# Optimization experiments

Measured on AMD Instinct MI355X. Metric: run time of the kernel, lower is better.

The kernel has to match this reference:

```python
import jax, jax.numpy as jnp
import numpy as np

EPS = 1e-3  # nn.LayerNorm(eps=0.001)
PADDING = 0.0


def setup_inputs() -> dict:
    key = jax.random.key(0)
    k1, k2, k3, k4 = jax.random.split(key, 4)
    N, M, K3, C_IN, C_OUT, B = 200000, 40000, 27, 64, 128, 4
    features = jax.random.normal(k1, (N, C_IN), dtype=jnp.float32)
    center_coors = jax.random.normal(k2, (M, 3), dtype=jnp.float32)
    voxel_idx = jax.random.randint(k3, (M, K3), 0, N, dtype=jnp.int64)
    num_list = jnp.full((B,), M // B, dtype=jnp.int32)
    W = jax.random.normal(k4, (K3 * C_IN, C_OUT), dtype=jnp.float32) * 1e-4
    gamma = jnp.ones((C_OUT,), dtype=jnp.float32)
    beta = jnp.zeros((C_OUT,), dtype=jnp.float32)
    return {
        "features": features,
        "center_coors": center_coors,
        "voxel_idx": voxel_idx,
        "num_list": num_list,
        "W": W,
        "gamma": gamma,
        "beta": beta,
        "num_keypoints": 2048,
    }


def _block(features, voxel_idx, W, gamma, beta):
    M, K3 = voxel_idx.shape
    C_in = features.shape[1]
    # voxel neighbor gather; negative idx -> padding value
    gathered = features[jnp.clip(voxel_idx, 0, features.shape[0] - 1)]  # [M, K3, C_in]
    gathered = jnp.where(voxel_idx[..., None] < 0, PADDING, gathered)
    flat = gathered.reshape(M, K3 * C_in)
    out = flat @ W  # [M, C_out]
    # LayerNorm over channel dim (per-batch loop in torch is mathematically
    # identical to a single row-wise LayerNorm)
    mu = jnp.mean(out, axis=-1, keepdims=True)
    var = jnp.mean(jnp.square(out - mu), axis=-1, keepdims=True)
    out = (out - mu) / jnp.sqrt(var + EPS) * gamma + beta
    return jax.nn.relu(out)


def _resample(out_features, center_coors, num_list, num_keypoints):
    B = num_list.shape[0]
    K = num_keypoints
    accum = jnp.cumsum(num_list)
    offsets = jnp.concatenate([jnp.zeros((1,), accum.dtype), accum[:-1]])  # [B]
    j = jnp.arange(K, dtype=jnp.int32)  # [K]
    end = jnp.minimum(num_list, jnp.int32(K))  # [B]
    valid = j[None, :] < end[:, None]  # [B, K]
    src = jnp.clip(offsets[:, None] + j[None, :], 0, out_features.shape[0] - 1)  # [B, K]
    res_feat = jnp.where(valid[..., None], out_features[src], 0.0)  # [B, K, C]
    res_xyz = jnp.where(valid[..., None], center_coors[src], 0.0)  # [B, K, 3]
    # replicate original quirk: segments 0..B-2 get batch index 1..B-1, last stays 0
    bid = jnp.arange(B, dtype=jnp.float32)
    col0 = jnp.where(bid < B - 1, bid + 1.0, 0.0)  # [B]
    col0 = jnp.broadcast_to(col0[:, None, None], (B, K, 1))
    res_coor = jnp.concatenate([col0, res_xyz], axis=-1)  # [B, K, 4]
    C = out_features.shape[1]
    return res_feat.reshape(B * K, C), res_coor.reshape(B * K, 4)


def reference(features, center_coors, voxel_idx, num_list, W, gamma, beta, num_keypoints):
    out = _block(features, voxel_idx, W, gamma, beta)
    point_features, point_coords = _resample(out, center_coors, num_list, num_keypoints)
    return point_features, point_coords
```

## Files before the change

### kernel.cpp

```cpp
#include <hip/hip_runtime.h>
#include <hip/hip_bf16.h>
#include <stdint.h>
#include <stddef.h>

#define TM 16
#define CIN 64
#define NK3 27
#define NK3P 28
#define COUT 128
#define EPS_LN 1e-3f
#define KCH  (NK3 * CIN / 32)
#define KCHP (NK3P * CIN / 32)
#define NT   (COUT / 16)
#define NPAIR (NK3P / 2)

typedef __attribute__((ext_vector_type(8))) short   short8;
typedef __attribute__((ext_vector_type(4))) float   floatx4;
typedef __attribute__((ext_vector_type(4))) unsigned short ushort4v;

__device__ __forceinline__ unsigned short f2b(float f) {
    union { float f; unsigned int i; } v;
    v.f = f;
    unsigned int i = v.i;
    return (unsigned short)((i + 0x7fffu + ((i >> 16) & 1u)) >> 16);
}

__global__ __launch_bounds__(256) void pack_w(const float* __restrict__ Wm,
                                              unsigned short* __restrict__ pk) {
    int slot = blockIdx.x * 256 + threadIdx.x;
    int l  = slot & 63;
    int kk = (slot >> 6) % KCHP;
    int nt = slot / (64 * KCHP);
    short8 v = {0, 0, 0, 0, 0, 0, 0, 0};
    if (kk < KCH) {
        int q = l >> 4, n = l & 15;
        const float* src = Wm + (size_t)(kk * 32 + q * 8) * COUT + nt * 16 + n;
        #pragma unroll
        for (int j = 0; j < 8; ++j)
            v[j] = (short)f2b(src[(size_t)j * COUT]);
    }
    *(short8*)(pk + (size_t)slot * 8) = v;
}

__global__ __launch_bounds__(256) void dpc_mfma(
    const float* __restrict__ features,
    const float* __restrict__ center,
    const int* __restrict__ voxel_idx,
    const int* __restrict__ num_list,
    const unsigned short* __restrict__ pk,
    const float* __restrict__ gamma_,
    const float* __restrict__ beta_,
    float* __restrict__ out_feat,
    float* __restrict__ out_coor,
    int N, int M, int B, int K, int Rtot)
{
    __shared__ int s_flags;
    __shared__ int s_vid[TM][NK3P];
    __shared__ int s_src[TM];
    __shared__ int s_valid[TM];
    __shared__ __align__(16) unsigned short s_a[2][2048];
    __shared__ float s_c[TM][COUT + 4];

    const int t  = threadIdx.x;
    const int R0 = blockIdx.x * TM;

    if (t == 0) {
        int f = 0;
        bool v64 = true;
        for (int j = 1; j < 128; j += 2) {
            if (voxel_idx[j] != 0) { v64 = false; break; }
        }
        if (v64) f |= 1;
        bool n64 = false;
        if (B >= 2) {
            n64 = (num_list[1] == 0) && (num_list[0] != 0);
            if (B >= 4) n64 = n64 && (num_list[3] == 0);
        }
        if (n64) f |= 2;
        s_flags = f;
    }
    __syncthreads();
    const bool vidx64 = (s_flags & 1) != 0;
    const bool nl64   = (s_flags & 2) != 0;

    if (t < TM) {
        int r = R0 + t;
        int src = 0, valid = 0;
        if (r < Rtot) {
            int b = r / K;
            int j = r - b * K;
            int offs = 0, nlb = 0;
            for (int i = 0; i < B; ++i) {
                int v = nl64 ? num_list[2 * i] : num_list[i];
                if (i < b) offs += v;
                if (i == b) nlb = v;
            }
            int end = nlb < K ? nlb : K;
            valid = (j < end) ? 1 : 0;
            src = offs + j;
            if (src < 0) src = 0;
            if (src > M - 1) src = M - 1;
        }
        s_src[t] = src;
        s_valid[t] = valid;
    }
    __syncthreads();

    if (t < TM * 4) {
        int i = t >> 2, comp = t & 3;
        int r = R0 + i;
        if (r < Rtot) {
            float val;
            if (comp == 0) {
                int b = r / K;
                val = (b < B - 1) ? (float)(b + 1) : 0.0f;
            } else {
                val = s_valid[i] ? center[(size_t)s_src[i] * 3 + comp - 1] : 0.0f;
            }
            out_coor[(size_t)r * 4 + comp] = val;
        }
    }

    for (int lin = t; lin < TM * NK3P; lin += 256) {
        int i = lin / NK3P;
        int k = lin - i * NK3P;
        int v = -1;
        if (k < NK3) {
            size_t e = (size_t)s_src[i] * NK3 + k;
            v = vidx64 ? voxel_idx[2 * e] : voxel_idx[e];
        }
        s_vid[i][k] = v;
    }
    __syncthreads();

    const int m  = t >> 4;
    const int c0 = (t & 15) * 4;
    const int chunk = c0 >> 5;
    const int q4    = (c0 & 31) >> 3;
    const int j0    = c0 & 7;
    const int aoff  = chunk * 512 + (q4 * 16 + m) * 8 + j0;

    auto gatherf4 = [&](int kc) -> float4 {
        int idx = s_vid[m][kc];
        float4 r = make_float4(0.f, 0.f, 0.f, 0.f);
        if (idx >= 0) {
            if (idx > N - 1) idx = N - 1;
            r = *(const float4*)(features + (size_t)idx * CIN + c0);
        }
        return r;
    };
    auto stash = [&](int buf, int sub, float4 v) {
        ushort4v u;
        u[0] = f2b(v.x); u[1] = f2b(v.y); u[2] = f2b(v.z); u[3] = f2b(v.w);
        *(ushort4v*)&s_a[buf][sub * 1024 + aoff] = u;
    };

    const int w    = t >> 6;
    const int lane = t & 63;
    const int nt0 = 2 * w, nt1 = 2 * w + 1;

    auto loadB = [&](int nt, int kk) -> short8 {
        return *(const short8*)(pk + ((size_t)(nt * KCHP + kk) * 64 + lane) * 8);
    };

    floatx4 acc0 = {0.f, 0.f, 0.f, 0.f};
    floatx4 acc1 = {0.f, 0.f, 0.f, 0.f};

    stash(0, 0, gatherf4(0));
    stash(0, 1, gatherf4(1));
    short8 bb[8];
    #pragma unroll
    for (int c = 0; c < 4; ++c) {
        bb[2 * c]     = loadB(nt0, c);
        bb[2 * c + 1] = loadB(nt1, c);
    }
    __syncthreads();

    for (int p = 0; p < NPAIR; ++p) {
        const int  buf = p & 1;
        const bool hn  = (p + 1 < NPAIR);

        float4 n0, n1;
        if (hn) { n0 = gatherf4(2 * p + 2); n1 = gatherf4(2 * p + 3); }
        short8 nb[8];
        if (hn) {
            #pragma unroll
            for (int c = 0; c < 4; ++c) {
                nb[2 * c]     = loadB(nt0, 4 * (p + 1) + c);
                nb[2 * c + 1] = loadB(nt1, 4 * (p + 1) + c);
            }
        }

        const short8 a0 = *(const short8*)&s_a[buf][           lane * 8];
        const short8 a1 = *(const short8*)&s_a[buf][ 512 +     lane * 8];
        const short8 a2 = *(const short8*)&s_a[buf][1024 +     lane * 8];
        const short8 a3 = *(const short8*)&s_a[buf][1536 +     lane * 8];

        acc0 = __builtin_amdgcn_mfma_f32_16x16x32_bf16(a0, bb[0], acc0, 0, 0, 0);
        acc1 = __builtin_amdgcn_mfma_f32_16x16x32_bf16(a0, bb[1], acc1, 0, 0, 0);
        acc0 = __builtin_amdgcn_mfma_f32_16x16x32_bf16(a1, bb[2], acc0, 0, 0, 0);
        acc1 = __builtin_amdgcn_mfma_f32_16x16x32_bf16(a1, bb[3], acc1, 0, 0, 0);
        acc0 = __builtin_amdgcn_mfma_f32_16x16x32_bf16(a2, bb[4], acc0, 0, 0, 0);
        acc1 = __builtin_amdgcn_mfma_f32_16x16x32_bf16(a2, bb[5], acc1, 0, 0, 0);
        acc0 = __builtin_amdgcn_mfma_f32_16x16x32_bf16(a3, bb[6], acc0, 0, 0, 0);
        acc1 = __builtin_amdgcn_mfma_f32_16x16x32_bf16(a3, bb[7], acc1, 0, 0, 0);

        if (hn) {
            stash(buf ^ 1, 0, n0);
            stash(buf ^ 1, 1, n1);
        }
        __syncthreads();
        if (hn) {
            #pragma unroll
            for (int i = 0; i < 8; ++i) bb[i] = nb[i];
        }
    }

    {
        const int q = lane >> 4, n = lane & 15;
        #pragma unroll
        for (int reg = 0; reg < 4; ++reg) {
            s_c[q * 4 + reg][nt0 * 16 + n] = acc0[reg];
            s_c[q * 4 + reg][nt1 * 16 + n] = acc1[reg];
        }
    }
    __syncthreads();

    const int h  = t >> 6;
    const int c2 = (t & 63) * 2;
    const float g0  = gamma_[c2];
    const float g1  = gamma_[c2 + 1];
    const float be0 = beta_[c2];
    const float be1 = beta_[c2 + 1];

    #pragma unroll
    for (int i = 0; i < 4; ++i) {
        int row = h * 4 + i;
        float a0 = s_c[row][c2];
        float a1 = s_c[row][c2 + 1];
        float s  = a0 + a1;
        float ss = a0 * a0 + a1 * a1;
        #pragma unroll
        for (int mm = 1; mm < 64; mm <<= 1) {
            s  += __shfl_xor(s,  mm, 64);
            ss += __shfl_xor(ss, mm, 64);
        }
        float mu   = s * (1.0f / COUT);
        float var  = ss * (1.0f / COUT) - mu * mu;
        float rstd = rsqrtf(var + EPS_LN);
        float v0 = (a0 - mu) * rstd * g0 + be0;
        float v1 = (a1 - mu) * rstd * g1 + be1;
        v0 = fmaxf(v0, 0.f);
        v1 = fmaxf(v1, 0.f);
        if (!s_valid[row]) { v0 = 0.f; v1 = 0.f; }
        int r = R0 + row;
        if (r < Rtot) {
            out_feat[(size_t)r * COUT + c2]     = v0;
            out_feat[(size_t)r * COUT + c2 + 1] = v1;
        }
    }
}

extern "C" void kernel_launch(void* const* d_in, const int* in_sizes, int n_in,
                              void* d_out, int out_size, void* d_ws, size_t ws_size,
                              hipStream_t stream) {
    const float* features = (const float*)d_in[0];
    const float* center   = (const float*)d_in[1];
    const int*   vidx     = (const int*)d_in[2];
    const int*   num_list = (const int*)d_in[3];
    const float* Wm       = (const float*)d_in[4];
    const float* gamma_   = (const float*)d_in[5];
    const float* beta_    = (const float*)d_in[6];

    const int B    = in_sizes[3];
    const int Cout = in_sizes[5];
    const int M    = in_sizes[1] / 3;
    const int K3v  = in_sizes[2] / M;
    const int Cin  = (in_sizes[4] / Cout) / K3v;
    const int N    = in_sizes[0] / Cin;
    const int Rtot = out_size / (Cout + 4);
    const int K    = Rtot / B;

    float* out_feat = (float*)d_out;
    float* out_coor = out_feat + (size_t)Rtot * Cout;
    unsigned short* pk = (unsigned short*)d_ws;

    const int pack_grid = (NT * KCHP * 64) / 256;
    pack_w<<<dim3(pack_grid), dim3(256), 0, stream>>>(Wm, pk);

    const int grid = (Rtot + TM - 1) / TM;
    dpc_mfma<<<dim3(grid), dim3(256), 0, stream>>>(
        features, center, vidx, num_list, pk, gamma_, beta_,
        out_feat, out_coor, N, M, B, K, Rtot);
}
```

Before: 113.2 us.

## Split the K dimension across blocks and reduce partials in a separate LayerNorm kernel

The gather-GEMM is split four ways along the 27-neighbour reduction dimension, so each tile launches four blocks that write fp32 partial sums to workspace. A new kernel sums the partials, applies LayerNorm and ReLU, and writes the coordinates. The input-width detection flags move into the weight-pack kernel and use a wave ballot instead of a serial loop in every block. This gives four times as many blocks for a small problem (8192 rows, 512 tiles), in exchange for an extra launch and a round trip of partial results through global memory. The Rtot bounds checks on the output writes were removed, so correctness depends on Rtot being a multiple of the 16-row tile.

```diff
diff --git a/kernel.cpp b/kernel.cpp
--- a/kernel.cpp
+++ b/kernel.cpp
@@ -12,7 +12,9 @@
 #define KCH  (NK3 * CIN / 32)
 #define KCHP (NK3P * CIN / 32)
 #define NT   (COUT / 16)
-#define NPAIR (NK3P / 2)
+#define SPLIT 4
+#define KPB  (NK3P / SPLIT)
+#define PK_BYTES (NT * KCHP * 64 * 8 * 2)
 
 typedef __attribute__((ext_vector_type(8))) short   short8;
 typedef __attribute__((ext_vector_type(4))) float   floatx4;
@@ -26,8 +28,27 @@
 }
 
 __global__ __launch_bounds__(256) void pack_w(const float* __restrict__ Wm,
-                                              unsigned short* __restrict__ pk) {
-    int slot = blockIdx.x * 256 + threadIdx.x;
+                                              const int* __restrict__ voxel_idx,
+                                              const int* __restrict__ num_list,
+                                              int Bc,
+                                              unsigned short* __restrict__ pk,
+                                              int* __restrict__ flags) {
+    const int t = threadIdx.x;
+    if (blockIdx.x == 0 && t < 64) {
+        int wv = voxel_idx[2 * t + 1];
+        unsigned long long nz = __ballot(wv != 0);
+        if (t == 0) {
+            int f = (nz == 0ULL) ? 1 : 0;
+            bool n64 = false;
+            if (Bc >= 2) {
+                n64 = (num_list[1] == 0) && (num_list[0] != 0);
+                if (Bc >= 4) n64 = n64 && (num_list[3] == 0);
+            }
+            if (n64) f |= 2;
+            flags[0] = f;
+        }
+    }
+    int slot = blockIdx.x * 256 + t;
     int l  = slot & 63;
     int kk = (slot >> 6) % KCHP;
     int nt = slot / (64 * KCHP);
@@ -42,46 +63,158 @@
     *(short8*)(pk + (size_t)slot * 8) = v;
 }
 
-__global__ __launch_bounds__(256) void dpc_mfma(
+__global__ __launch_bounds__(256) void dpc_gemm_split(
     const float* __restrict__ features,
-    const float* __restrict__ center,
     const int* __restrict__ voxel_idx,
     const int* __restrict__ num_list,
     const unsigned short* __restrict__ pk,
+    const int* __restrict__ flags,
+    float* __restrict__ partial,
+    int N, int M, int B, int K, int Rtot)
+{
+    const int tile  = blockIdx.x / SPLIT;
+    const int split = blockIdx.x - tile * SPLIT;
+    const int R0 = tile * TM;
+    const int t  = threadIdx.x;
+
+    __shared__ int s_flags;
+    __shared__ int s_src[TM];
+    __shared__ int s_vid[TM][KPB];
+    __shared__ __align__(16) unsigned short s_a[2][1024];
+
+    if (t == 0) s_flags = flags[0];
+    __syncthreads();
+    const bool vidx64 = (s_flags & 1) != 0;
+    const bool nl64   = (s_flags & 2) != 0;
+
+    if (t < TM) {
+        int r = R0 + t;
+        int src = 0;
+        if (r < Rtot) {
+            int b = r / K;
+            int j = r - b * K;
+            int offs = 0;
+            for (int i = 0; i < B; ++i) {
+                int v = nl64 ? num_list[2 * i] : num_list[i];
+                if (i < b) offs += v;
+            }
+            src = offs + j;
+            if (src < 0) src = 0;
+            if (src > M - 1) src = M - 1;
+        }
+        s_src[t] = src;
+    }
+    __syncthreads();
+
+    for (int lin = t; lin < TM * KPB; lin += 256) {
+        int i = lin / KPB;
+        int k = lin - i * KPB;
+        int kc = split * KPB + k;
+        int v = -1;
+        if (kc < NK3) {
+            size_t e = (size_t)s_src[i] * NK3 + kc;
+            v = vidx64 ? voxel_idx[2 * e] : voxel_idx[e];
+        }
+        s_vid[i][k] = v;
+    }
+
+    const int m  = t >> 4;
+    const int c0 = (t & 15) * 4;
+    const int chunk = c0 >> 5;
+    const int q4    = (c0 & 31) >> 3;
+    const int j0    = c0 & 7;
+    const int aoff  = chunk * 512 + (q4 * 16 + m) * 8 + j0;
+
+    auto gatherf4 = [&](int k) -> float4 {
+        int idx = s_vid[m][k];
+        float4 r = make_float4(0.f, 0.f, 0.f, 0.f);
+        if (idx >= 0) {
+            if (idx > N - 1) idx = N - 1;
+            r = *(const float4*)(features + (size_t)idx * CIN + c0);
+        }
+        return r;
+    };
+    auto stash = [&](int buf, float4 v) {
+        ushort4v u;
+        u[0] = f2b(v.x); u[1] = f2b(v.y); u[2] = f2b(v.z); u[3] = f2b(v.w);
+        *(ushort4v*)&s_a[buf][aoff] = u;
+    };
+
+    const int w    = t >> 6;
+    const int lane = t & 63;
+    const int nt0 = 2 * w, nt1 = 2 * w + 1;
+    auto loadB = [&](int nt, int kk) -> short8 {
+        return *(const short8*)(pk + ((size_t)(nt * KCHP + kk) * 64 + lane) * 8);
+    };
+
+    floatx4 acc0 = {0.f, 0.f, 0.f, 0.f};
+    floatx4 acc1 = {0.f, 0.f, 0.f, 0.f};
+
+    __syncthreads();
+    stash(0, gatherf4(0));
+    const int kkb = split * KPB * 2;
+    short8 bb[4];
+    bb[0] = loadB(nt0, kkb); bb[1] = loadB(nt1, kkb);
+    bb[2] = loadB(nt0, kkb + 1); bb[3] = loadB(nt1, kkb + 1);
+    __syncthreads();
+
+    for (int i = 0; i < KPB; ++i) {
+        const int  buf = i & 1;
+        const bool hn  = (i + 1 < KPB);
+        float4 pref;
+        short8 nb[4];
+        if (hn) {
+            pref = gatherf4(i + 1);
+            const int kk = kkb + 2 * (i + 1);
+            nb[0] = loadB(nt0, kk); nb[1] = loadB(nt1, kk);
+            nb[2] = loadB(nt0, kk + 1); nb[3] = loadB(nt1, kk + 1);
+        }
+        const short8 a0 = *(const short8*)&s_a[buf][      lane * 8];
+        const short8 a1 = *(const short8*)&s_a[buf][512 + lane * 8];
+
+        acc0 = __builtin_amdgcn_mfma_f32_16x16x32_bf16(a0, bb[0], acc0, 0, 0, 0);
+        acc1 = __builtin_amdgcn_mfma_f32_16x16x32_bf16(a0, bb[1], acc1, 0, 0, 0);
+        acc0 = __builtin_amdgcn_mfma_f32_16x16x32_bf16(a1, bb[2], acc0, 0, 0, 0);
+        acc1 = __builtin_amdgcn_mfma_f32_16x16x32_bf16(a1, bb[3], acc1, 0, 0, 0);
+
+        if (hn) stash(buf ^ 1, pref);
+        __syncthreads();
+        if (hn) { bb[0] = nb[0]; bb[1] = nb[1]; bb[2] = nb[2]; bb[3] = nb[3]; }
+    }
+
+    {
+        const int q = lane >> 4, n = lane & 15;
+        float* base = partial + (size_t)split * Rtot * COUT + (size_t)R0 * COUT;
+        #pragma unroll
+        for (int reg = 0; reg < 4; ++reg) {
+            int row = q * 4 + reg;
+            base[(size_t)row * COUT + nt0 * 16 + n] = acc0[reg];
+            base[(size_t)row * COUT + nt1 * 16 + n] = acc1[reg];
+        }
+    }
+}
+
+__global__ __launch_bounds__(256) void dpc_reduce_ln(
+    const float* __restrict__ partial,
+    const float* __restrict__ center,
+    const int* __restrict__ num_list,
+    const int* __restrict__ flags,
     const float* __restrict__ gamma_,
     const float* __restrict__ beta_,
     float* __restrict__ out_feat,
     float* __restrict__ out_coor,
-    int N, int M, int B, int K, int Rtot)
+    int M, int B, int K, int Rtot)
 {
+    const int t  = threadIdx.x;
+    const int R0 = blockIdx.x * TM;
+
     __shared__ int s_flags;
-    __shared__ int s_vid[TM][NK3P];
     __shared__ int s_src[TM];
     __shared__ int s_valid[TM];
-    __shared__ __align__(16) unsigned short s_a[2][2048];
-    __shared__ float s_c[TM][COUT + 4];
-
-    const int t  = threadIdx.x;
-    const int R0 = blockIdx.x * TM;
-
-    if (t == 0) {
-        int f = 0;
-        bool v64 = true;
-        for (int j = 1; j < 128; j += 2) {
-            if (voxel_idx[j] != 0) { v64 = false; break; }
-        }
-        if (v64) f |= 1;
-        bool n64 = false;
-        if (B >= 2) {
-            n64 = (num_list[1] == 0) && (num_list[0] != 0);
-            if (B >= 4) n64 = n64 && (num_list[3] == 0);
-        }
-        if (n64) f |= 2;
-        s_flags = f;
-    }
-    __syncthreads();
-    const bool vidx64 = (s_flags & 1) != 0;
-    const bool nl64   = (s_flags & 2) != 0;
+
+    if (t == 0) s_flags = flags[0];
+    __syncthreads();
+    const bool nl64 = (s_flags & 2) != 0;
 
     if (t < TM) {
         int r = R0 + t;
@@ -121,111 +254,6 @@
         }
     }
 
-    for (int lin = t; lin < TM * NK3P; lin += 256) {
-        int i = lin / NK3P;
-        int k = lin - i * NK3P;
-        int v = -1;
-        if (k < NK3) {
-            size_t e = (size_t)s_src[i] * NK3 + k;
-            v = vidx64 ? voxel_idx[2 * e] : voxel_idx[e];
-        }
-        s_vid[i][k] = v;
-    }
-    __syncthreads();
-
-    const int m  = t >> 4;
-    const int c0 = (t & 15) * 4;
-    const int chunk = c0 >> 5;
-    const int q4    = (c0 & 31) >> 3;
-    const int j0    = c0 & 7;
-    const int aoff  = chunk * 512 + (q4 * 16 + m) * 8 + j0;
-
-    auto gatherf4 = [&](int kc) -> float4 {
-        int idx = s_vid[m][kc];
-        float4 r = make_float4(0.f, 0.f, 0.f, 0.f);
-        if (idx >= 0) {
-            if (idx > N - 1) idx = N - 1;
-            r = *(const float4*)(features + (size_t)idx * CIN + c0);
-        }
-        return r;
-    };
-    auto stash = [&](int buf, int sub, float4 v) {
-        ushort4v u;
-        u[0] = f2b(v.x); u[1] = f2b(v.y); u[2] = f2b(v.z); u[3] = f2b(v.w);
-        *(ushort4v*)&s_a[buf][sub * 1024 + aoff] = u;
-    };
-
-    const int w    = t >> 6;
-    const int lane = t & 63;
-    const int nt0 = 2 * w, nt1 = 2 * w + 1;
-
-    auto loadB = [&](int nt, int kk) -> short8 {
-        return *(const short8*)(pk + ((size_t)(nt * KCHP + kk) * 64 + lane) * 8);
-    };
-
-    floatx4 acc0 = {0.f, 0.f, 0.f, 0.f};
-    floatx4 acc1 = {0.f, 0.f, 0.f, 0.f};
-
-    stash(0, 0, gatherf4(0));
-    stash(0, 1, gatherf4(1));
-    short8 bb[8];
-    #pragma unroll
-    for (int c = 0; c < 4; ++c) {
-        bb[2 * c]     = loadB(nt0, c);
-        bb[2 * c + 1] = loadB(nt1, c);
-    }
-    __syncthreads();
-
-    for (int p = 0; p < NPAIR; ++p) {
-        const int  buf = p & 1;
-        const bool hn  = (p + 1 < NPAIR);
-
-        float4 n0, n1;
-        if (hn) { n0 = gatherf4(2 * p + 2); n1 = gatherf4(2 * p + 3); }
-        short8 nb[8];
-        if (hn) {
-            #pragma unroll
-            for (int c = 0; c < 4; ++c) {
-                nb[2 * c]     = loadB(nt0, 4 * (p + 1) + c);
-                nb[2 * c + 1] = loadB(nt1, 4 * (p + 1) + c);
-            }
-        }
-
-        const short8 a0 = *(const short8*)&s_a[buf][           lane * 8];
-        const short8 a1 = *(const short8*)&s_a[buf][ 512 +     lane * 8];
-        const short8 a2 = *(const short8*)&s_a[buf][1024 +     lane * 8];
-        const short8 a3 = *(const short8*)&s_a[buf][1536 +     lane * 8];
-
-        acc0 = __builtin_amdgcn_mfma_f32_16x16x32_bf16(a0, bb[0], acc0, 0, 0, 0);
-        acc1 = __builtin_amdgcn_mfma_f32_16x16x32_bf16(a0, bb[1], acc1, 0, 0, 0);
-        acc0 = __builtin_amdgcn_mfma_f32_16x16x32_bf16(a1, bb[2], acc0, 0, 0, 0);
-        acc1 = __builtin_amdgcn_mfma_f32_16x16x32_bf16(a1, bb[3], acc1, 0, 0, 0);
-        acc0 = __builtin_amdgcn_mfma_f32_16x16x32_bf16(a2, bb[4], acc0, 0, 0, 0);
-        acc1 = __builtin_amdgcn_mfma_f32_16x16x32_bf16(a2, bb[5], acc1, 0, 0, 0);
-        acc0 = __builtin_amdgcn_mfma_f32_16x16x32_bf16(a3, bb[6], acc0, 0, 0, 0);
-        acc1 = __builtin_amdgcn_mfma_f32_16x16x32_bf16(a3, bb[7], acc1, 0, 0, 0);
-
-        if (hn) {
-            stash(buf ^ 1, 0, n0);
-            stash(buf ^ 1, 1, n1);
-        }
-        __syncthreads();
-        if (hn) {
-            #pragma unroll
-            for (int i = 0; i < 8; ++i) bb[i] = nb[i];
-        }
-    }
-
-    {
-        const int q = lane >> 4, n = lane & 15;
-        #pragma unroll
-        for (int reg = 0; reg < 4; ++reg) {
-            s_c[q * 4 + reg][nt0 * 16 + n] = acc0[reg];
-            s_c[q * 4 + reg][nt1 * 16 + n] = acc1[reg];
-        }
-    }
-    __syncthreads();
-
     const int h  = t >> 6;
     const int c2 = (t & 63) * 2;
     const float g0  = gamma_[c2];
@@ -236,8 +264,13 @@
     #pragma unroll
     for (int i = 0; i < 4; ++i) {
         int row = h * 4 + i;
-        float a0 = s_c[row][c2];
-        float a1 = s_c[row][c2 + 1];
+        int r = R0 + row;
+        float a0 = 0.f, a1 = 0.f;
+        #pragma unroll
+        for (int s = 0; s < SPLIT; ++s) {
+            const float2 v = *(const float2*)(partial + ((size_t)s * Rtot + r) * COUT + c2);
+            a0 += v.x; a1 += v.y;
+        }
         float s  = a0 + a1;
         float ss = a0 * a0 + a1 * a1;
         #pragma unroll
@@ -253,11 +286,8 @@
         v0 = fmaxf(v0, 0.f);
         v1 = fmaxf(v1, 0.f);
         if (!s_valid[row]) { v0 = 0.f; v1 = 0.f; }
-        int r = R0 + row;
-        if (r < Rtot) {
-            out_feat[(size_t)r * COUT + c2]     = v0;
-            out_feat[(size_t)r * COUT + c2 + 1] = v1;
-        }
+        out_feat[(size_t)r * COUT + c2]     = v0;
+        out_feat[(size_t)r * COUT + c2 + 1] = v1;
     }
 }
 
@@ -283,13 +313,19 @@
 
     float* out_feat = (float*)d_out;
     float* out_coor = out_feat + (size_t)Rtot * Cout;
-    unsigned short* pk = (unsigned short*)d_ws;
+
+    unsigned short* pk   = (unsigned short*)d_ws;
+    int*   flags   = (int*)((char*)d_ws + PK_BYTES);
+    float* partial = (float*)((char*)d_ws + PK_BYTES + 16);
 
     const int pack_grid = (NT * KCHP * 64) / 256;
-    pack_w<<<dim3(pack_grid), dim3(256), 0, stream>>>(Wm, pk);
-
-    const int grid = (Rtot + TM - 1) / TM;
-    dpc_mfma<<<dim3(grid), dim3(256), 0, stream>>>(
-        features, center, vidx, num_list, pk, gamma_, beta_,
-        out_feat, out_coor, N, M, B, K, Rtot);
-}
+    pack_w<<<dim3(pack_grid), dim3(256), 0, stream>>>(Wm, vidx, num_list, B, pk, flags);
+
+    const int tiles = (Rtot + TM - 1) / TM;
+    dpc_gemm_split<<<dim3(tiles * SPLIT), dim3(256), 0, stream>>>(
+        features, vidx, num_list, pk, flags, partial, N, M, B, K, Rtot);
+
+    dpc_reduce_ln<<<dim3(tiles), dim3(256), 0, stream>>>(
+        partial, center, num_list, flags, gamma_, beta_,
+        out_feat, out_coor, M, B, K, Rtot);
+}
```

After: 118.7 us. 4.9% more time.

## Deepen gather pipeline to triple-buffered LDS and precompute index-width flags

Applied to the files above, without the earlier changes.

The main kernel now keeps the neighbour gather two stages ahead, using a three-slot shared-memory ring instead of double buffering. This gives global gather latency more time to hide behind the MFMA work. The index-width and num_list-width detection moves out of every block's serial thread-0 loop into the weight-packing kernel, which uses a wave ballot and writes a flag to workspace that the main kernel reads. In exchange, the block uses more LDS and registers for the extra prefetched values, which may reduce occupancy.

```diff
diff --git a/kernel.cpp b/kernel.cpp
--- a/kernel.cpp
+++ b/kernel.cpp
@@ -13,6 +13,7 @@
 #define KCHP (NK3P * CIN / 32)
 #define NT   (COUT / 16)
 #define NPAIR (NK3P / 2)
+#define PK_BYTES (NT * KCHP * 64 * 8 * 2)
 
 typedef __attribute__((ext_vector_type(8))) short   short8;
 typedef __attribute__((ext_vector_type(4))) float   floatx4;
@@ -26,8 +27,27 @@
 }
 
 __global__ __launch_bounds__(256) void pack_w(const float* __restrict__ Wm,
-                                              unsigned short* __restrict__ pk) {
-    int slot = blockIdx.x * 256 + threadIdx.x;
+                                              const int* __restrict__ voxel_idx,
+                                              const int* __restrict__ num_list,
+                                              int Bc,
+                                              unsigned short* __restrict__ pk,
+                                              int* __restrict__ flags) {
+    const int t = threadIdx.x;
+    if (blockIdx.x == 0 && t < 64) {
+        int wv = voxel_idx[2 * t + 1];
+        unsigned long long nz = __ballot(wv != 0);
+        if (t == 0) {
+            int f = (nz == 0ULL) ? 1 : 0;
+            bool n64 = false;
+            if (Bc >= 2) {
+                n64 = (num_list[1] == 0) && (num_list[0] != 0);
+                if (Bc >= 4) n64 = n64 && (num_list[3] == 0);
+            }
+            if (n64) f |= 2;
+            flags[0] = f;
+        }
+    }
+    int slot = blockIdx.x * 256 + t;
     int l  = slot & 63;
     int kk = (slot >> 6) % KCHP;
     int nt = slot / (64 * KCHP);
@@ -48,40 +68,25 @@
     const int* __restrict__ voxel_idx,
     const int* __restrict__ num_list,
     const unsigned short* __restrict__ pk,
+    const int* __restrict__ flags,
     const float* __restrict__ gamma_,
     const float* __restrict__ beta_,
     float* __restrict__ out_feat,
     float* __restrict__ out_coor,
     int N, int M, int B, int K, int Rtot)
 {
-    __shared__ int s_flags;
     __shared__ int s_vid[TM][NK3P];
     __shared__ int s_src[TM];
     __shared__ int s_valid[TM];
-    __shared__ __align__(16) unsigned short s_a[2][2048];
+    __shared__ __align__(16) unsigned short s_a[3][2048];
     __shared__ float s_c[TM][COUT + 4];
 
     const int t  = threadIdx.x;
     const int R0 = blockIdx.x * TM;
 
-    if (t == 0) {
-        int f = 0;
-        bool v64 = true;
-        for (int j = 1; j < 128; j += 2) {
-            if (voxel_idx[j] != 0) { v64 = false; break; }
-        }
-        if (v64) f |= 1;
-        bool n64 = false;
-        if (B >= 2) {
-            n64 = (num_list[1] == 0) && (num_list[0] != 0);
-            if (B >= 4) n64 = n64 && (num_list[3] == 0);
-        }
-        if (n64) f |= 2;
-        s_flags = f;
-    }
-    __syncthreads();
-    const bool vidx64 = (s_flags & 1) != 0;
-    const bool nl64   = (s_flags & 2) != 0;
+    const int fl = flags[0];
+    const bool vidx64 = (fl & 1) != 0;
+    const bool nl64   = (fl & 2) != 0;
 
     if (t < TM) {
         int r = R0 + t;
@@ -158,7 +163,6 @@
     const int w    = t >> 6;
     const int lane = t & 63;
     const int nt0 = 2 * w, nt1 = 2 * w + 1;
-
     auto loadB = [&](int nt, int kk) -> short8 {
         return *(const short8*)(pk + ((size_t)(nt * KCHP + kk) * 64 + lane) * 8);
     };
@@ -168,6 +172,8 @@
 
     stash(0, 0, gatherf4(0));
     stash(0, 1, gatherf4(1));
+    float4 cA0 = gatherf4(2);
+    float4 cA1 = gatherf4(3);
     short8 bb[8];
     #pragma unroll
     for (int c = 0; c < 4; ++c) {
@@ -177,24 +183,26 @@
     __syncthreads();
 
     for (int p = 0; p < NPAIR; ++p) {
-        const int  buf = p & 1;
-        const bool hn  = (p + 1 < NPAIR);
-
-        float4 n0, n1;
-        if (hn) { n0 = gatherf4(2 * p + 2); n1 = gatherf4(2 * p + 3); }
+        const bool hasC = (p + 1 < NPAIR);
+        const bool hasN = (p + 2 < NPAIR);
+
+        float4 nA0, nA1;
+        if (hasN) { nA0 = gatherf4(2 * p + 4); nA1 = gatherf4(2 * p + 5); }
         short8 nb[8];
-        if (hn) {
+        if (hasC) {
+            const int kk = 4 * (p + 1);
             #pragma unroll
             for (int c = 0; c < 4; ++c) {
-                nb[2 * c]     = loadB(nt0, 4 * (p + 1) + c);
-                nb[2 * c + 1] = loadB(nt1, 4 * (p + 1) + c);
+                nb[2 * c]     = loadB(nt0, kk + c);
+                nb[2 * c + 1] = loadB(nt1, kk + c);
             }
         }
 
-        const short8 a0 = *(const short8*)&s_a[buf][           lane * 8];
-        const short8 a1 = *(const short8*)&s_a[buf][ 512 +     lane * 8];
-        const short8 a2 = *(const short8*)&s_a[buf][1024 +     lane * 8];
-        const short8 a3 = *(const short8*)&s_a[buf][1536 +     lane * 8];
+        const int buf = p % 3;
+        const short8 a0 = *(const short8*)&s_a[buf][       lane * 8];
+        const short8 a1 = *(const short8*)&s_a[buf][ 512 + lane * 8];
+        const short8 a2 = *(const short8*)&s_a[buf][1024 + lane * 8];
+        const short8 a3 = *(const short8*)&s_a[buf][1536 + lane * 8];
 
         acc0 = __builtin_amdgcn_mfma_f32_16x16x32_bf16(a0, bb[0], acc0, 0, 0, 0);
         acc1 = __builtin_amdgcn_mfma_f32_16x16x32_bf16(a0, bb[1], acc1, 0, 0, 0);
@@ -205,23 +213,25 @@
         acc0 = __builtin_amdgcn_mfma_f32_16x16x32_bf16(a3, bb[6], acc0, 0, 0, 0);
         acc1 = __builtin_amdgcn_mfma_f32_16x16x32_bf16(a3, bb[7], acc1, 0, 0, 0);
 
-        if (hn) {
-            stash(buf ^ 1, 0, n0);
-            stash(buf ^ 1, 1, n1);
+        if (hasC) {
+            const int wb = (p + 1) % 3;
+            stash(wb, 0, cA0);
+            stash(wb, 1, cA1);
         }
         __syncthreads();
-        if (hn) {
+        if (hasC) {
             #pragma unroll
             for (int i = 0; i < 8; ++i) bb[i] = nb[i];
         }
+        if (hasN) { cA0 = nA0; cA1 = nA1; }
     }
 
     {
-        const int q = lane >> 4, n = lane & 15;
+        const int cq = lane >> 4, n = lane & 15;
         #pragma unroll
         for (int reg = 0; reg < 4; ++reg) {
-            s_c[q * 4 + reg][nt0 * 16 + n] = acc0[reg];
-            s_c[q * 4 + reg][nt1 * 16 + n] = acc1[reg];
+            s_c[cq * 4 + reg][nt0 * 16 + n] = acc0[reg];
+            s_c[cq * 4 + reg][nt1 * 16 + n] = acc1[reg];
         }
     }
     __syncthreads();
@@ -283,13 +293,15 @@
 
     float* out_feat = (float*)d_out;
     float* out_coor = out_feat + (size_t)Rtot * Cout;
+
     unsigned short* pk = (unsigned short*)d_ws;
+    int* flags = (int*)((char*)d_ws + PK_BYTES);
 
     const int pack_grid = (NT * KCHP * 64) / 256;
-    pack_w<<<dim3(pack_grid), dim3(256), 0, stream>>>(Wm, pk);
-
-    const int grid = (Rtot + TM - 1) / TM;
-    dpc_mfma<<<dim3(grid), dim3(256), 0, stream>>>(
-        features, center, vidx, num_list, pk, gamma_, beta_,
+    pack_w<<<dim3(pack_grid), dim3(256), 0, stream>>>(Wm, vidx, num_list, B, pk, flags);
+
+    const int tiles = (Rtot + TM - 1) / TM;
+    dpc_mfma<<<dim3(tiles), dim3(256), 0, stream>>>(
+        features, center, vidx, num_list, pk, flags, gamma_, beta_,
         out_feat, out_coor, N, M, B, K, Rtot);
 }
```

Measured after the change: 112.2 us. No clear change (-0.9%).
